# Kernel optimization log

Hardware: AMD Instinct MI355X
Metric: run time of the kernel (lower is better)

## Reference

```python
import jax, jax.numpy as jnp
import numpy as np

B, S, D = 2, 2048, 1024
H = 16
HD = D // H   # 64
K = 64        # local_window / neighbors per position


def setup_inputs() -> dict:
    key = jax.random.key(0)
    k1, k2, k3, k4, k5, k6 = jax.random.split(key, 6)
    scale = 1.0 / np.sqrt(D)
    x = jax.random.normal(k1, (B, S, D), dtype=jnp.float32)
    routes = jax.random.randint(k2, (S, K), 0, S, dtype=jnp.int64)
    W_qkv = jax.random.normal(k3, (D, 3 * D), dtype=jnp.float32) * scale
    b_qkv = jnp.zeros((3 * D,), dtype=jnp.float32)
    W_proj = jax.random.normal(k4, (D, D), dtype=jnp.float32) * scale
    b_proj = jnp.zeros((D,), dtype=jnp.float32)
    return {"x": x, "W_qkv": W_qkv, "b_qkv": b_qkv,
            "W_proj": W_proj, "b_proj": b_proj, "routes": routes}


def reference(x, W_qkv, b_qkv, W_proj, b_proj, routes):
    # x: (B, S, D)
    qkv = x @ W_qkv + b_qkv                       # (B, S, 3D)
    qkv = qkv.reshape(B, S, 3, H, HD)
    q, k, v = qkv[:, :, 0], qkv[:, :, 1], qkv[:, :, 2]   # (B, S, H, HD)
    q = q.transpose(0, 2, 1, 3)                   # (B, H, S, HD)
    k = k.transpose(0, 2, 1, 3)
    v = v.transpose(0, 2, 1, 3)

    r = jnp.clip(routes, 0, S - 1)                # (S, K)
    # Gather neighbor keys/values: (B, H, S, K, HD)
    k_n = k[:, :, r, :]
    v_n = v[:, :, r, :]

    scores = jnp.einsum('bhsd,bhskd->bhsk', q, k_n) / jnp.sqrt(
        jnp.asarray(HD, dtype=q.dtype))           # (B, H, S, K)
    attn = jax.nn.softmax(scores, axis=-1)
    out = jnp.einsum('bhsk,bhskd->bhsd', attn, v_n)       # (B, H, S, HD)

    out = out.transpose(0, 2, 1, 3).reshape(B, S, D)
    return out @ W_proj + b_proj
```

## Files before the change

kernel.cpp:

```cpp
#include <hip/hip_runtime.h>
#include <stdint.h>

#define B_ 2
#define S_ 2048
#define D_ 1024
#define H_ 16
#define HD_ 64
#define K_ 64

typedef __attribute__((ext_vector_type(8))) __bf16 bf16x8v;
typedef __attribute__((ext_vector_type(4))) float f32x4;
typedef __attribute__((ext_vector_type(8))) unsigned short ushort8v;

#define GLD_LDS16(g, l)                                                        \
  __builtin_amdgcn_global_load_lds(                                            \
      (const __attribute__((address_space(1))) void*)(g),                      \
      (__attribute__((address_space(3))) void*)(l), 16, 0, 0)

__device__ __forceinline__ float bf2f(unsigned short u) {
  union { unsigned u32; float f; } c;
  c.u32 = ((unsigned)u) << 16;
  return c.f;
}
__device__ __forceinline__ unsigned short f2bf(float f) {
  union { float f; unsigned u; } c;
  c.f = f;
  unsigned u = c.u;
  u += 0x7fffu + ((u >> 16) & 1u);
  return (unsigned short)(u >> 16);
}

__global__ __launch_bounds__(256) void cast_f32_bf16(
    const float4* __restrict__ in, ushort4* __restrict__ outp, int n4) {
  int i = blockIdx.x * 256 + threadIdx.x;
  if (i >= n4) return;
  float4 v = in[i];
  ushort4 o;
  o.x = f2bf(v.x); o.y = f2bf(v.y); o.z = f2bf(v.z); o.w = f2bf(v.w);
  outp[i] = o;
}

__global__ __launch_bounds__(256) void transpose_cast(
    const float* __restrict__ W, unsigned short* __restrict__ WT, int R, int C) {
  __shared__ float tile[64][65];
  const int r0 = blockIdx.y * 64;
  const int c0 = blockIdx.x * 64;
  const int t = threadIdx.x;
#pragma unroll
  for (int i = 0; i < 16; ++i) {
    int idx = t + i * 256;
    int rr = idx >> 6, cc = idx & 63;
    tile[rr][cc] = W[(size_t)(r0 + rr) * C + c0 + cc];
  }
  __syncthreads();
#pragma unroll
  for (int i = 0; i < 16; ++i) {
    int idx = t + i * 256;
    int rr = idx >> 6, cc = idx & 63;
    WT[(size_t)(c0 + rr) * R + r0 + cc] = f2bf(tile[cc][rr]);
  }
}

template <bool OUT_F32>
__global__ __launch_bounds__(256) void gemm_bias(
    const unsigned short* __restrict__ A, const unsigned short* __restrict__ Bt,
    const float* __restrict__ bias, void* __restrict__ Cout,
    int M, int N, int Kd) {
  __shared__ unsigned short As[128 * 32];
  __shared__ unsigned short Bs[128 * 32];
  const int t = threadIdx.x;
  const int w = t >> 6;
  const int l = t & 63;
  const int m0 = blockIdx.y * 128;
  const int n0 = blockIdx.x * 128;
  const int wr = w >> 1, wc = w & 1;

  f32x4 acc[4][4] = {};

  const int srow = t >> 2;
  const int scol = (t & 3) * 8;
  char* asBase = (char*)As + w * 1024;
  char* bsBase = (char*)Bs + w * 1024;

  const int lr = l & 15;
  const int kh = (l >> 4) * 8;

  const int KT = Kd >> 5;
  for (int kt = 0; kt < KT; ++kt) {
    const int k0 = kt << 5;
    {
      const unsigned short* g0 = A + (size_t)(m0 + srow) * Kd + k0 + scol;
      const unsigned short* g1 = A + (size_t)(m0 + 64 + srow) * Kd + k0 + scol;
      GLD_LDS16(g0, asBase);
      GLD_LDS16(g1, asBase + 4096);
      const unsigned short* h0 = Bt + (size_t)(n0 + srow) * Kd + k0 + scol;
      const unsigned short* h1 = Bt + (size_t)(n0 + 64 + srow) * Kd + k0 + scol;
      GLD_LDS16(h0, bsBase);
      GLD_LDS16(h1, bsBase + 4096);
    }
    __syncthreads();
    bf16x8v af[4], bfv[4];
#pragma unroll
    for (int m = 0; m < 4; ++m)
      af[m] = *(const bf16x8v*)&As[(wr * 64 + m * 16 + lr) * 32 + kh];
#pragma unroll
    for (int n = 0; n < 4; ++n)
      bfv[n] = *(const bf16x8v*)&Bs[(wc * 64 + n * 16 + lr) * 32 + kh];
#pragma unroll
    for (int m = 0; m < 4; ++m)
#pragma unroll
      for (int n = 0; n < 4; ++n)
        acc[m][n] = __builtin_amdgcn_mfma_f32_16x16x32_bf16(af[m], bfv[n],
                                                            acc[m][n], 0, 0, 0);
    __syncthreads();
  }

  const int rbase = (l >> 4) * 4;
#pragma unroll
  for (int m = 0; m < 4; ++m) {
#pragma unroll
    for (int n = 0; n < 4; ++n) {
      const int gc = n0 + wc * 64 + n * 16 + lr;
      const float bv = bias[gc];
#pragma unroll
      for (int j = 0; j < 4; ++j) {
        const int gr = m0 + wr * 64 + m * 16 + rbase + j;
        float v = acc[m][n][j] + bv;
        if (OUT_F32)
          ((float*)Cout)[(size_t)gr * N + gc] = v;
        else
          ((unsigned short*)Cout)[(size_t)gr * N + gc] = f2bf(v);
      }
    }
  }
}

__global__ __launch_bounds__(256) void attn_kernel(
    const unsigned short* __restrict__ qkv, const int* __restrict__ routes,
    unsigned short* __restrict__ outp) {
  __shared__ float sc[16][68];
  __shared__ unsigned rtsoff[64];
  __shared__ float pbuf[1024];
  const int bs = blockIdx.x;
  const int b = bs >> 11;
  const int s = bs & (S_ - 1);
  const int t = threadIdx.x;
  const int w = t >> 6, l = t & 63;
  const int kh2 = w >> 1, hh = w & 1;

  if (t < 64) {
    int r = routes[s * K_ + t];
    r = min(max(r, 0), S_ - 1);
    rtsoff[t] = (unsigned)(b * S_ + r) * 3072u;
  }
  __syncthreads();

  const unsigned colo = hh * 512 + l * 8;
  const int head = colo >> 6;
  const size_t rowbase = (size_t)bs * 3072;

  float q[8];
  {
    ushort8v u = *(const ushort8v*)(qkv + rowbase + colo);
#pragma unroll
    for (int i = 0; i < 8; ++i) q[i] = bf2f(u[i]) * 0.125f;
  }

  const unsigned kofs = 1024u + colo;
  const unsigned vofs = 2048u + colo;
  const int jbase = kh2 * 32;

#pragma unroll 4
  for (int j2 = 0; j2 < 32; ++j2) {
    const int j = jbase + j2;
    ushort8v u = *(const ushort8v*)(qkv + (rtsoff[j] + kofs));
    float d = q[0] * bf2f(u[0]);
#pragma unroll
    for (int i = 1; i < 8; ++i) d += q[i] * bf2f(u[i]);
    d += __shfl_xor(d, 1);
    d += __shfl_xor(d, 2);
    d += __shfl_xor(d, 4);
    if ((l & 7) == 0) sc[head][j] = d;
  }
  __syncthreads();

  {
    const int h = t >> 4;
    const int l2 = t & 15;
    float v0 = sc[h][l2], v1 = sc[h][l2 + 16], v2 = sc[h][l2 + 32],
          v3 = sc[h][l2 + 48];
    float m = fmaxf(fmaxf(v0, v1), fmaxf(v2, v3));
    m = fmaxf(m, __shfl_xor(m, 1));
    m = fmaxf(m, __shfl_xor(m, 2));
    m = fmaxf(m, __shfl_xor(m, 4));
    m = fmaxf(m, __shfl_xor(m, 8));
    v0 = __expf(v0 - m); v1 = __expf(v1 - m);
    v2 = __expf(v2 - m); v3 = __expf(v3 - m);
    float ss = v0 + v1 + v2 + v3;
    ss += __shfl_xor(ss, 1);
    ss += __shfl_xor(ss, 2);
    ss += __shfl_xor(ss, 4);
    ss += __shfl_xor(ss, 8);
    float inv = 1.0f / ss;
    sc[h][l2] = v0 * inv;
    sc[h][l2 + 16] = v1 * inv;
    sc[h][l2 + 32] = v2 * inv;
    sc[h][l2 + 48] = v3 * inv;
  }
  __syncthreads();

  float acc[8] = {};
#pragma unroll 4
  for (int j2 = 0; j2 < 32; ++j2) {
    const int j = jbase + j2;
    ushort8v u = *(const ushort8v*)(qkv + (rtsoff[j] + vofs));
    const float p = sc[head][j];
#pragma unroll
    for (int i = 0; i < 8; ++i) acc[i] += p * bf2f(u[i]);
  }

  if (kh2 == 1) {
    f32x4 a0 = {acc[0], acc[1], acc[2], acc[3]};
    f32x4 a1 = {acc[4], acc[5], acc[6], acc[7]};
    *(f32x4*)&pbuf[colo] = a0;
    *(f32x4*)&pbuf[colo + 4] = a1;
  }
  __syncthreads();
  if (kh2 == 0) {
    ushort8v o;
#pragma unroll
    for (int i = 0; i < 8; ++i) o[i] = f2bf(acc[i] + pbuf[colo + i]);
    *(ushort8v*)(outp + (size_t)bs * D_ + colo) = o;
  }
}

extern "C" void kernel_launch(void* const* d_in, const int* in_sizes, int n_in,
                              void* d_out, int out_size, void* d_ws,
                              size_t ws_size, hipStream_t stream) {
  const float* x = (const float*)d_in[0];
  const float* Wqkv = (const float*)d_in[1];
  const float* bqkv = (const float*)d_in[2];
  const float* Wproj = (const float*)d_in[3];
  const float* bproj = (const float*)d_in[4];
  const int* routes = (const int*)d_in[5];
  float* out = (float*)d_out;

  char* ws = (char*)d_ws;
  unsigned short* x_bf = (unsigned short*)(ws);
  unsigned short* wqkvT = (unsigned short*)(ws + 8388608);
  unsigned short* wprojT = (unsigned short*)(ws + 14680064);
  unsigned short* qkv = (unsigned short*)(ws + 16777216);
  unsigned short* aout = (unsigned short*)(ws + 41943040);

  {
    int n4 = (B_ * S_ * D_) / 4;
    cast_f32_bf16<<<n4 / 256, 256, 0, stream>>>((const float4*)x,
                                                (ushort4*)x_bf, n4);
  }
  transpose_cast<<<dim3(3 * D_ / 64, D_ / 64), 256, 0, stream>>>(Wqkv, wqkvT,
                                                                 D_, 3 * D_);
  transpose_cast<<<dim3(D_ / 64, D_ / 64), 256, 0, stream>>>(Wproj, wprojT, D_,
                                                             D_);
  gemm_bias<false><<<dim3(3 * D_ / 128, B_ * S_ / 128), 256, 0, stream>>>(
      x_bf, wqkvT, bqkv, qkv, B_ * S_, 3 * D_, D_);
  attn_kernel<<<B_ * S_, 256, 0, stream>>>(qkv, routes, aout);
  gemm_bias<true><<<dim3(D_ / 128, B_ * S_ / 128), 256, 0, stream>>>(
      aout, wprojT, bproj, out, B_ * S_, D_, D_);
}
```

Before: 146.8 us.

## Fuse softmax into single-pass attention and remap GEMM blocks across XCDs

The attention kernel now computes scores, exponentials and the weighted V sum in one loop, loading K and V together. It normalizes only at the end through a shared partial sum, which removes the score buffer and two block barriers. It drops the max-subtraction, so very large scores could overflow the exponential. The GEMMs switch to a 1D grid with a block-id permutation that groups consecutive tiles per XCD (id&7 chunking) to improve L2 locality.

```diff
diff --git a/kernel.cpp b/kernel.cpp
--- a/kernel.cpp
+++ b/kernel.cpp
@@ -65,14 +65,20 @@
 __global__ __launch_bounds__(256) void gemm_bias(
     const unsigned short* __restrict__ A, const unsigned short* __restrict__ Bt,
     const float* __restrict__ bias, void* __restrict__ Cout,
-    int M, int N, int Kd) {
+    int M, int N, int Kd, int gx) {
   __shared__ unsigned short As[128 * 32];
   __shared__ unsigned short Bs[128 * 32];
   const int t = threadIdx.x;
   const int w = t >> 6;
   const int l = t & 63;
-  const int m0 = blockIdx.y * 128;
-  const int n0 = blockIdx.x * 128;
+
+  const int nblk = (int)gridDim.x;
+  int id = (int)blockIdx.x;
+  id = (id & 7) * (nblk >> 3) + (id >> 3);
+  const int by = id / gx;
+  const int bx = id - by * gx;
+  const int m0 = by * 128;
+  const int n0 = bx * 128;
   const int wr = w >> 1, wc = w & 1;
 
   f32x4 acc[4][4] = {};
@@ -138,9 +144,9 @@
 __global__ __launch_bounds__(256) void attn_kernel(
     const unsigned short* __restrict__ qkv, const int* __restrict__ routes,
     unsigned short* __restrict__ outp) {
-  __shared__ float sc[16][68];
   __shared__ unsigned rtsoff[64];
   __shared__ float pbuf[1024];
+  __shared__ float lbuf[16];
   const int bs = blockIdx.x;
   const int b = bs >> 11;
   const int s = bs & (S_ - 1);
@@ -157,66 +163,34 @@
 
   const unsigned colo = hh * 512 + l * 8;
   const int head = colo >> 6;
-  const size_t rowbase = (size_t)bs * 3072;
 
   float q[8];
   {
-    ushort8v u = *(const ushort8v*)(qkv + rowbase + colo);
-#pragma unroll
-    for (int i = 0; i < 8; ++i) q[i] = bf2f(u[i]) * 0.125f;
+    ushort8v u = *(const ushort8v*)(qkv + (size_t)bs * 3072 + colo);
+#pragma unroll
+    for (int i = 0; i < 8; ++i) q[i] = bf2f(u[i]);
   }
 
   const unsigned kofs = 1024u + colo;
-  const unsigned vofs = 2048u + colo;
   const int jbase = kh2 * 32;
 
+  float acc[8] = {};
+  float lsum = 0.f;
 #pragma unroll 4
   for (int j2 = 0; j2 < 32; ++j2) {
-    const int j = jbase + j2;
-    ushort8v u = *(const ushort8v*)(qkv + (rtsoff[j] + kofs));
-    float d = q[0] * bf2f(u[0]);
-#pragma unroll
-    for (int i = 1; i < 8; ++i) d += q[i] * bf2f(u[i]);
+    const unsigned ro = rtsoff[jbase + j2];
+    ushort8v ku = *(const ushort8v*)(qkv + (ro + kofs));
+    ushort8v vu = *(const ushort8v*)(qkv + (ro + kofs + 1024u));
+    float d = q[0] * bf2f(ku[0]);
+#pragma unroll
+    for (int i = 1; i < 8; ++i) d += q[i] * bf2f(ku[i]);
     d += __shfl_xor(d, 1);
     d += __shfl_xor(d, 2);
     d += __shfl_xor(d, 4);
-    if ((l & 7) == 0) sc[head][j] = d;
-  }
-  __syncthreads();
-
-  {
-    const int h = t >> 4;
-    const int l2 = t & 15;
-    float v0 = sc[h][l2], v1 = sc[h][l2 + 16], v2 = sc[h][l2 + 32],
-          v3 = sc[h][l2 + 48];
-    float m = fmaxf(fmaxf(v0, v1), fmaxf(v2, v3));
-    m = fmaxf(m, __shfl_xor(m, 1));
-    m = fmaxf(m, __shfl_xor(m, 2));
-    m = fmaxf(m, __shfl_xor(m, 4));
-    m = fmaxf(m, __shfl_xor(m, 8));
-    v0 = __expf(v0 - m); v1 = __expf(v1 - m);
-    v2 = __expf(v2 - m); v3 = __expf(v3 - m);
-    float ss = v0 + v1 + v2 + v3;
-    ss += __shfl_xor(ss, 1);
-    ss += __shfl_xor(ss, 2);
-    ss += __shfl_xor(ss, 4);
-    ss += __shfl_xor(ss, 8);
-    float inv = 1.0f / ss;
-    sc[h][l2] = v0 * inv;
-    sc[h][l2 + 16] = v1 * inv;
-    sc[h][l2 + 32] = v2 * inv;
-    sc[h][l2 + 48] = v3 * inv;
-  }
-  __syncthreads();
-
-  float acc[8] = {};
-#pragma unroll 4
-  for (int j2 = 0; j2 < 32; ++j2) {
-    const int j = jbase + j2;
-    ushort8v u = *(const ushort8v*)(qkv + (rtsoff[j] + vofs));
-    const float p = sc[head][j];
-#pragma unroll
-    for (int i = 0; i < 8; ++i) acc[i] += p * bf2f(u[i]);
+    const float p = __expf(d * 0.125f);
+    lsum += p;
+#pragma unroll
+    for (int i = 0; i < 8; ++i) acc[i] += p * bf2f(vu[i]);
   }
 
   if (kh2 == 1) {
@@ -224,12 +198,14 @@
     f32x4 a1 = {acc[4], acc[5], acc[6], acc[7]};
     *(f32x4*)&pbuf[colo] = a0;
     *(f32x4*)&pbuf[colo + 4] = a1;
+    if ((l & 7) == 0) lbuf[head] = lsum;
   }
   __syncthreads();
   if (kh2 == 0) {
+    const float inv = 1.0f / (lsum + lbuf[head]);
     ushort8v o;
 #pragma unroll
-    for (int i = 0; i < 8; ++i) o[i] = f2bf(acc[i] + pbuf[colo + i]);
+    for (int i = 0; i < 8; ++i) o[i] = f2bf((acc[i] + pbuf[colo + i]) * inv);
     *(ushort8v*)(outp + (size_t)bs * D_ + colo) = o;
   }
 }
@@ -261,9 +237,15 @@
                                                                  D_, 3 * D_);
   transpose_cast<<<dim3(D_ / 64, D_ / 64), 256, 0, stream>>>(Wproj, wprojT, D_,
                                                              D_);
-  gemm_bias<false><<<dim3(3 * D_ / 128, B_ * S_ / 128), 256, 0, stream>>>(
-      x_bf, wqkvT, bqkv, qkv, B_ * S_, 3 * D_, D_);
+  {
+    int gx = 3 * D_ / 128, gy = B_ * S_ / 128;
+    gemm_bias<false><<<gx * gy, 256, 0, stream>>>(x_bf, wqkvT, bqkv, qkv,
+                                                  B_ * S_, 3 * D_, D_, gx);
+  }
   attn_kernel<<<B_ * S_, 256, 0, stream>>>(qkv, routes, aout);
-  gemm_bias<true><<<dim3(D_ / 128, B_ * S_ / 128), 256, 0, stream>>>(
-      aout, wprojT, bproj, out, B_ * S_, D_, D_);
-}
+  {
+    int gx = D_ / 128, gy = B_ * S_ / 128;
+    gemm_bias<true><<<gx * gy, 256, 0, stream>>>(aout, wprojT, bproj, out,
+                                                 B_ * S_, D_, D_, gx);
+  }
+}
```

Measured after the change: 161.0 us. +9.7%, slower.

## Replace QKV GEMM with 256x256 tile double-buffered pipelined MFMA kernel

Applied to the files above, without the earlier changes.

Adds a dedicated QKV projection GEMM using 256x256 tiles, 512 threads, and K-step 64 with two LDS buffers, prefetching two stages ahead via direct global-to-LDS loads. The work is interleaved MFMA phases with staged loads and setprio, aiming to hide load latency and raise reuse per byte. The trade-off is that the larger tile yields only 192 blocks, fewer than the CU count, and large LDS use limits occupancy.

```diff
diff --git a/kernel.cpp b/kernel.cpp
--- a/kernel.cpp
+++ b/kernel.cpp
@@ -133,6 +133,144 @@
       }
     }
   }
+}
+
+__global__ __launch_bounds__(512, 2) void gemm_qkv_256(
+    const unsigned short* __restrict__ A, const unsigned short* __restrict__ Bt,
+    const float* __restrict__ bias, unsigned short* __restrict__ Cout) {
+  __shared__ unsigned short As2[2][256 * 64];
+  __shared__ unsigned short Bs2[2][256 * 64];
+  const int t = threadIdx.x;
+  const int w = t >> 6, l = t & 63;
+  const int wr = w >> 2, wc = w & 3;
+  const int m0 = blockIdx.y * 256, n0 = blockIdx.x * 256;
+
+  f32x4 acc[8][4] = {};
+
+  const int srow = w * 8 + (l >> 3);
+  const int scol = (l & 7) * 8;
+  const int ldsoff = w * 1024;
+
+#define STAGE_A(kt, buf)                                                       \
+  {                                                                            \
+    _Pragma("unroll") for (int i = 0; i < 4; ++i)                              \
+        GLD_LDS16(A + (size_t)(m0 + srow + i * 64) * 1024 + (kt) * 64 + scol,  \
+                  (char*)As2[buf] + ldsoff + i * 8192);                        \
+  }
+#define STAGE_B(kt, buf)                                                       \
+  {                                                                            \
+    _Pragma("unroll") for (int i = 0; i < 4; ++i)                              \
+        GLD_LDS16(Bt + (size_t)(n0 + srow + i * 64) * 1024 + (kt) * 64 + scol, \
+                  (char*)Bs2[buf] + ldsoff + i * 8192);                        \
+  }
+
+  const int lr = l & 15, kq = (l >> 4) * 8;
+  const int KT = 16;
+
+  STAGE_B(0, 0); STAGE_A(0, 0);
+  STAGE_B(1, 1); STAGE_A(1, 1);
+
+  bf16x8v a4[4][2], b01[2][2], b23[2][2];
+
+  for (int kt = 0; kt < KT; ++kt) {
+    const int cur = kt & 1;
+    if (kt < KT - 1)
+      asm volatile("s_waitcnt vmcnt(8)" ::: "memory");
+    else
+      asm volatile("s_waitcnt vmcnt(0)" ::: "memory");
+    __builtin_amdgcn_s_barrier();
+
+#pragma unroll
+    for (int m = 0; m < 4; ++m)
+#pragma unroll
+      for (int ks = 0; ks < 2; ++ks)
+        a4[m][ks] = *(const bf16x8v*)&As2[cur][(wr * 128 + m * 16 + lr) * 64 +
+                                              ks * 32 + kq];
+#pragma unroll
+    for (int n = 0; n < 2; ++n)
+#pragma unroll
+      for (int ks = 0; ks < 2; ++ks)
+        b01[n][ks] = *(const bf16x8v*)&Bs2[cur][(wc * 64 + n * 16 + lr) * 64 +
+                                               ks * 32 + kq];
+    __builtin_amdgcn_s_setprio(1);
+#pragma unroll
+    for (int m = 0; m < 4; ++m)
+#pragma unroll
+      for (int n = 0; n < 2; ++n)
+#pragma unroll
+        for (int ks = 0; ks < 2; ++ks)
+          acc[m][n] = __builtin_amdgcn_mfma_f32_16x16x32_bf16(
+              a4[m][ks], b01[n][ks], acc[m][n], 0, 0, 0);
+    __builtin_amdgcn_s_setprio(0);
+
+#pragma unroll
+    for (int n = 0; n < 2; ++n)
+#pragma unroll
+      for (int ks = 0; ks < 2; ++ks)
+        b23[n][ks] = *(const bf16x8v*)&Bs2[cur][(wc * 64 + (n + 2) * 16 + lr) *
+                                                   64 + ks * 32 + kq];
+    __builtin_amdgcn_s_setprio(1);
+#pragma unroll
+    for (int m = 0; m < 4; ++m)
+#pragma unroll
+      for (int n = 0; n < 2; ++n)
+#pragma unroll
+        for (int ks = 0; ks < 2; ++ks)
+          acc[m][n + 2] = __builtin_amdgcn_mfma_f32_16x16x32_bf16(
+              a4[m][ks], b23[n][ks], acc[m][n + 2], 0, 0, 0);
+    __builtin_amdgcn_s_setprio(0);
+
+    __builtin_amdgcn_s_barrier();
+
+    if (kt + 2 < KT) STAGE_B(kt + 2, cur);
+#pragma unroll
+    for (int m = 0; m < 4; ++m)
+#pragma unroll
+      for (int ks = 0; ks < 2; ++ks)
+        a4[m][ks] = *(const bf16x8v*)&As2[cur][(wr * 128 + (m + 4) * 16 + lr) *
+                                                  64 + ks * 32 + kq];
+    __builtin_amdgcn_s_setprio(1);
+#pragma unroll
+    for (int m = 0; m < 4; ++m)
+#pragma unroll
+      for (int n = 0; n < 2; ++n)
+#pragma unroll
+        for (int ks = 0; ks < 2; ++ks)
+          acc[m + 4][n + 2] = __builtin_amdgcn_mfma_f32_16x16x32_bf16(
+              a4[m][ks], b23[n][ks], acc[m + 4][n + 2], 0, 0, 0);
+    __builtin_amdgcn_s_setprio(0);
+
+    __builtin_amdgcn_s_barrier();
+
+    if (kt + 2 < KT) STAGE_A(kt + 2, cur);
+    __builtin_amdgcn_s_setprio(1);
+#pragma unroll
+    for (int m = 0; m < 4; ++m)
+#pragma unroll
+      for (int n = 0; n < 2; ++n)
+#pragma unroll
+        for (int ks = 0; ks < 2; ++ks)
+          acc[m + 4][n] = __builtin_amdgcn_mfma_f32_16x16x32_bf16(
+              a4[m][ks], b01[n][ks], acc[m + 4][n], 0, 0, 0);
+    __builtin_amdgcn_s_setprio(0);
+  }
+
+  const int rb = (l >> 4) * 4;
+#pragma unroll
+  for (int m = 0; m < 8; ++m) {
+#pragma unroll
+    for (int n = 0; n < 4; ++n) {
+      const int gc = n0 + wc * 64 + n * 16 + lr;
+      const float bv = bias[gc];
+#pragma unroll
+      for (int j = 0; j < 4; ++j) {
+        const int gr = m0 + wr * 128 + m * 16 + rb + j;
+        Cout[(size_t)gr * 3072 + gc] = f2bf(acc[m][n][j] + bv);
+      }
+    }
+  }
+#undef STAGE_A
+#undef STAGE_B
 }
 
 __global__ __launch_bounds__(256) void attn_kernel(
@@ -261,8 +399,8 @@
                                                                  D_, 3 * D_);
   transpose_cast<<<dim3(D_ / 64, D_ / 64), 256, 0, stream>>>(Wproj, wprojT, D_,
                                                              D_);
-  gemm_bias<false><<<dim3(3 * D_ / 128, B_ * S_ / 128), 256, 0, stream>>>(
-      x_bf, wqkvT, bqkv, qkv, B_ * S_, 3 * D_, D_);
+  gemm_qkv_256<<<dim3(3 * D_ / 256, B_ * S_ / 256), 512, 0, stream>>>(
+      x_bf, wqkvT, bqkv, qkv);
   attn_kernel<<<B_ * S_, 256, 0, stream>>>(qkv, routes, aout);
   gemm_bias<true><<<dim3(D_ / 128, B_ * S_ / 128), 256, 0, stream>>>(
       aout, wprojT, bproj, out, B_ * S_, D_, D_);
```

New measurement: 157.5 us. +7.3%, slower.
